# Kernel optimization log

Hardware: AMD Instinct MI355X
Metric: run time of the kernel (lower is better)

Reference implementation:

```python
import jax, jax.numpy as jnp
import numpy as np

B, T, L, M = 64, 2000, 400, 80
SIGMA_FACTOR = 0.05
SIGMA_CAP = 10.0
SIGMA_MIN = 1.5
WARMUP_STEPS = 10000
GLOBAL_STEP = 0  # fresh loss module -> progress = 0
ENTROPY_TARGET = 3.5
ATTN_W_START = 1.0
ATTN_W_MIN = 0.2
EPS = 1e-8


def setup_inputs() -> dict:
    key = jax.random.key(0)
    ks = jax.random.split(key, 8)
    mel_out_postnet = jax.random.normal(ks[0], (B, T, M), jnp.float32)
    mel_out = jax.random.normal(ks[1], (B, T, M), jnp.float32)
    gate_out = jax.random.normal(ks[2], (B, T), jnp.float32)
    # alignments: stacked per-step attention, row-normalized like real softmax outputs
    a = jax.random.uniform(ks[3], (B, T, L), jnp.float32)
    alignments = a / jnp.sum(a, axis=-1, keepdims=True)
    mel_target = jax.random.normal(ks[4], (B, T, M), jnp.float32)
    gate_target = jnp.round(jax.random.uniform(ks[5], (B, T), jnp.float32))
    mel_lengths = jax.random.randint(ks[6], (B,), T // 2, T + 1, jnp.int32).at[0].set(T)
    text_lengths = jax.random.randint(ks[7], (B,), L // 2, L + 1, jnp.int32).at[0].set(L)
    return {
        "mel_out_postnet": mel_out_postnet, "mel_out": mel_out, "gate_out": gate_out,
        "alignments": alignments, "mel_target": mel_target, "gate_target": gate_target,
        "mel_lengths": mel_lengths, "text_lengths": text_lengths,
    }


def _diagonal_target(text_lengths):
    # sigma per batch element; global_step=0 -> progress=0 -> sigma = init_sigma
    init_sigma = jnp.clip(text_lengths.astype(jnp.float32) * SIGMA_FACTOR, 3.0, SIGMA_CAP)
    progress = min(1.0, GLOBAL_STEP / float(WARMUP_STEPS))
    sigma = init_sigma - (init_sigma - SIGMA_MIN) * progress  # [B]
    t = jnp.arange(T, dtype=jnp.int32)  # decoder steps
    Lb = text_lengths[:, None]  # [B,1]
    # expected_pos = min(int(t*Lb/T), Lb-1); positive ints -> integer floor div matches trunc
    exp_pos = jnp.minimum((t[None, :] * Lb) // T, Lb - 1).astype(jnp.float32)  # [B,T]
    pos = jnp.arange(L, dtype=jnp.float32)  # [L]
    z = (pos[None, None, :] - exp_pos[:, :, None]) / sigma[:, None, None]
    g = jnp.exp(-0.5 * z * z)  # [B,T,L]
    valid = (pos[None, None, :] < text_lengths[:, None, None].astype(jnp.float32))
    g = g * valid
    return g / (jnp.sum(g, axis=-1, keepdims=True) + EPS)


def reference(mel_out_postnet, mel_out, gate_out, alignments, mel_target,
              gate_target, mel_lengths, text_lengths):
    # masked L1 on mel (mel_target already [B,T,M], matching the torch transpose)
    valid = (jnp.arange(T)[None, :] < mel_lengths[:, None])[:, :, None]  # [B,T,1]
    vf = valid.astype(jnp.float32)
    n_valid = jnp.sum(vf) * M
    mel_loss_1 = jnp.sum(jnp.abs(mel_out - mel_target) * vf) / n_valid
    mel_loss_2 = jnp.sum(jnp.abs(mel_out_postnet - mel_target) * vf) / n_valid
    loss_mel = mel_loss_1 + mel_loss_2

    # BCEWithLogits, mean reduction (stable form)
    x, z_t = gate_out, gate_target
    loss_gate = jnp.mean(jnp.maximum(x, 0.0) - x * z_t + jnp.log1p(jnp.exp(-jnp.abs(x))))

    # guided-attention KL against diagonal Gaussian target
    target = _diagonal_target(text_lengths)  # [B,T,L]
    attn_safe = jnp.maximum(alignments, EPS)
    log_pred = jnp.log(attn_safe)
    kl_pw = jnp.where(target > 0.0, target * (jnp.log(jnp.maximum(target, EPS)) - log_pred), 0.0)
    attention_kl = jnp.sum(kl_pw) / B / T  # batchmean then / T_dec
    attention_kl = jnp.minimum(attention_kl, 150.0)

    # entropy-gated attention weight (python-float in torch -> stop_gradient)
    attn_entropy = jnp.mean(-jnp.sum(attn_safe * log_pred, axis=2))
    ratio = jnp.maximum(attn_entropy / ENTROPY_TARGET, 0.0)
    weight = jnp.where(attn_entropy <= ENTROPY_TARGET,
                       jnp.maximum(ATTN_W_MIN, ATTN_W_START * ratio),
                       ATTN_W_START)
    weight = jax.lax.stop_gradient(weight)

    total_loss = loss_mel + loss_gate + weight * attention_kl
    return (total_loss, loss_mel, loss_gate, attention_kl)
```

## Files before the change

kernel.cpp:

```cpp
#include <hip/hip_runtime.h>
#include <cstddef>
#include <cstdint>

#define B_ 64
#define T_ 2000
#define L_ 400
#define M_ 80
#define EPSF 1e-8f
#define LOG2_EPSF -26.575424759098897f
#define LN2 0.6931471805599453

#define NBLK 2048
#define BT_ (B_ * T_)
#define NTHREADS (NBLK * 256)
#define NWAVES (NBLK * 4)
#define L4_ 100
#define TAIL_LANES 36
#define N4_ (B_ * T_ * (M_ / 4))
#define NCH_ (N4_ / 64)
#define MAXK 16
#define MELK 5

typedef float vf4 __attribute__((ext_vector_type(4)));

#define LOG2F(x) __builtin_amdgcn_logf(x)
#define EXP2F(x) __builtin_amdgcn_exp2f(x)

__device__ __forceinline__ float waveReduce(float v) {
#pragma unroll
  for (int m = 32; m >= 1; m >>= 1) v += __shfl_xor(v, m, 64);
  return v;
}

__global__ __launch_bounds__(256) void fused_kernel(
    const vf4* __restrict__ mo, const vf4* __restrict__ mp,
    const vf4* __restrict__ mt, const float* __restrict__ gx,
    const float* __restrict__ gz, const float* __restrict__ align,
    const int* __restrict__ mel_lengths, const int* __restrict__ text_lengths,
    double* __restrict__ ws) {
  __shared__ int sh_ml[B_];
  __shared__ int sh_tl[B_];
  if (threadIdx.x < B_) {
    sh_ml[threadIdx.x] = mel_lengths[threadIdx.x];
    sh_tl[threadIdx.x] = text_lengths[threadIdx.x];
  }
  __syncthreads();

  const int tid = blockIdx.x * 256 + threadIdx.x;
  const int lane = threadIdx.x & 63;
  const int wib = threadIdx.x >> 6;
  const int waveId = blockIdx.x * 4 + wib;

  float mel_acc = 0.f, gate_acc = 0.f, kl_acc = 0.f, ent2_acc = 0.f;

  if (tid < BT_) {
    float xv = gx[tid], z = gz[tid];
    gate_acc = fmaxf(xv, 0.f) - xv * z + log1pf(__expf(-fabsf(xv)));
  }

  const float4* a4 = reinterpret_cast<const float4*>(align);
  const float fl0 = (float)(4 * lane);

  float4 c0, c1 = make_float4(0.f, 0.f, 0.f, 0.f);
  {
    const float4* r = a4 + (size_t)waveId * L4_;
    c0 = r[lane];
    if (lane < TAIL_LANES) c1 = r[64 + lane];
  }

#pragma unroll 1
  for (int k = 0; k < MAXK; ++k) {
    const int p = waveId + k * NWAVES;
    const bool pv = (p < BT_);

    float4 n0 = make_float4(0.f, 0.f, 0.f, 0.f), n1 = n0;
    const int pn = p + NWAVES;
    if (pn < BT_) {
      const float4* r = a4 + (size_t)pn * L4_;
      n0 = r[lane];
      if (lane < TAIL_LANES) n1 = r[64 + lane];
    }

    vf4 ma, mb, md;
    int mi = 0;
    bool mv = false;
    if (k < MELK) {
      int ch = waveId + k * NWAVES;
      mv = (ch < NCH_);
      if (mv) {
        mi = ch * 64 + lane;
        ma = __builtin_nontemporal_load(&mo[mi]);
        mb = __builtin_nontemporal_load(&mp[mi]);
        md = __builtin_nontemporal_load(&mt[mi]);
      }
    }

    if (pv) {
      int b = p / T_;
      int t = p - b * T_;
      int Lb = sh_tl[b];
      float sigma = fminf(fmaxf((float)Lb * 0.05f, 3.0f), 10.0f);
      float invsig = 1.0f / sigma;
      int epi = t * Lb / T_;
      int lim = Lb - 1;
      if (epi > lim) epi = lim;
      float ep = (float)epi;
      float cg = -0.7213475204444817f * invsig * invsig;
      float d0 = fl0 - ep;
      float d1 = d0 + 256.f;

      float S = 0.f, W2 = 0.f;
      float gs[8];
#pragma unroll
      for (int j = 4; j < 8; ++j) gs[j] = 0.f;

      {
        const float av[4] = {c0.x, c0.y, c0.z, c0.w};
#pragma unroll
        for (int j = 0; j < 4; ++j) {
          float as = fmaxf(av[j], EPSF);
          float lp2 = LOG2F(as);
          ent2_acc = fmaf(-as, lp2, ent2_acc);
          float dj = d0 + (float)j;
          float e2 = dj * dj * cg;
          float gv = EXP2F(e2);
          gv = ((4 * lane + j) < Lb) ? gv : 0.f;
          gs[j] = gv;
          S += gv;
          W2 = fmaf(gv, lp2, W2);
        }
      }
      const bool c1w = (256.f - ep) < 13.6f * sigma;
      if (lane < TAIL_LANES) {
        const float av[4] = {c1.x, c1.y, c1.z, c1.w};
#pragma unroll
        for (int j = 0; j < 4; ++j) {
          float as = fmaxf(av[j], EPSF);
          float lp2 = LOG2F(as);
          ent2_acc = fmaf(-as, lp2, ent2_acc);
          if (c1w) {
            float dj = d1 + (float)j;
            float e2 = dj * dj * cg;
            float gv = EXP2F(e2);
            gv = ((256 + 4 * lane + j) < Lb) ? gv : 0.f;
            gs[4 + j] = gv;
            S += gv;
            W2 = fmaf(gv, lp2, W2);
          }
        }
      }

      float St = waveReduce(S);
      float Se = St + EPSF;
      float inv = 1.0f / Se;
      float lSe2 = LOG2F(Se);

      float K2 = 0.f;
#pragma unroll
      for (int j = 0; j < 4; ++j) {
        float dj = d0 + (float)j;
        float e2 = dj * dj * cg;
        K2 = fmaf(gs[j], fmaxf(e2 - lSe2, LOG2_EPSF), K2);
      }
      if (c1w) {
#pragma unroll
        for (int j = 0; j < 4; ++j) {
          float dj = d1 + (float)j;
          float e2 = dj * dj * cg;
          K2 = fmaf(gs[4 + j], fmaxf(e2 - lSe2, LOG2_EPSF), K2);
        }
      }
      kl_acc = fmaf(inv, K2 - W2, kl_acc);
    }

    if (mv) {
      int row = mi / 20;
      int b2 = row / T_;
      int t2 = row - b2 * T_;
      float s8 = fabsf(ma.x - md.x) + fabsf(ma.y - md.y) + fabsf(ma.z - md.z) +
                 fabsf(ma.w - md.w) + fabsf(mb.x - md.x) + fabsf(mb.y - md.y) +
                 fabsf(mb.z - md.z) + fabsf(mb.w - md.w);
      mel_acc += (t2 < sh_ml[b2]) ? s8 : 0.f;
    }

    c0 = n0;
    c1 = n1;
  }

  float w0 = waveReduce(mel_acc);
  float w1 = waveReduce(gate_acc);
  float w2 = waveReduce(kl_acc);
  float w3 = waveReduce(ent2_acc);
  __shared__ double sh[4][4];
  if (lane == 0) {
    sh[wib][0] = (double)w0; sh[wib][1] = (double)w1;
    sh[wib][2] = (double)w2; sh[wib][3] = (double)w3;
  }
  __syncthreads();
  if (threadIdx.x == 0) {
    ws[blockIdx.x]            = sh[0][0] + sh[1][0] + sh[2][0] + sh[3][0];
    ws[NBLK + blockIdx.x]     = sh[0][1] + sh[1][1] + sh[2][1] + sh[3][1];
    ws[2 * NBLK + blockIdx.x] = sh[0][2] + sh[1][2] + sh[2][2] + sh[3][2];
    ws[3 * NBLK + blockIdx.x] = sh[0][3] + sh[1][3] + sh[2][3] + sh[3][3];
  }
}

__device__ double segSum(const double* __restrict__ p, int n, double* sh) {
  double a = 0.0;
  for (int i = threadIdx.x; i < n; i += 256) a += p[i];
  sh[threadIdx.x] = a;
  __syncthreads();
  for (int s = 128; s > 0; s >>= 1) {
    if ((int)threadIdx.x < s) sh[threadIdx.x] += sh[threadIdx.x + s];
    __syncthreads();
  }
  double r = sh[0];
  __syncthreads();
  return r;
}

__global__ __launch_bounds__(256) void finalize_kernel(
    const double* __restrict__ ws, const int* __restrict__ mel_lengths,
    float* __restrict__ out) {
  __shared__ double sh[256];
  double mel_sum  = segSum(ws, NBLK, sh);
  double gate_sum = segSum(ws + NBLK, NBLK, sh);
  double kl_sum   = segSum(ws + 2 * NBLK, NBLK, sh);
  double ent_sum  = segSum(ws + 3 * NBLK, NBLK, sh);
  if (threadIdx.x == 0) {
    long nv = 0;
    for (int b = 0; b < B_; ++b) nv += mel_lengths[b];
    double n_valid = (double)nv * (double)M_;
    float loss_mel  = (float)(mel_sum / n_valid);
    float loss_gate = (float)(gate_sum / (double)(B_ * T_));
    float kl  = (float)(kl_sum * LN2 / (double)(B_ * T_));
    kl = fminf(kl, 150.0f);
    float ent = (float)(ent_sum * LN2 / (double)(B_ * T_));
    float ratio = fmaxf(ent / 3.5f, 0.0f);
    float weight = (ent <= 3.5f) ? fmaxf(0.2f, 1.0f * ratio) : 1.0f;
    out[0] = loss_mel + loss_gate + weight * kl;
    out[1] = loss_mel;
    out[2] = loss_gate;
    out[3] = kl;
  }
}

extern "C" void kernel_launch(void* const* d_in, const int* in_sizes, int n_in,
                              void* d_out, int out_size, void* d_ws, size_t ws_size,
                              hipStream_t stream) {
  const float* mel_out_postnet = (const float*)d_in[0];
  const float* mel_out         = (const float*)d_in[1];
  const float* gate_out        = (const float*)d_in[2];
  const float* alignments      = (const float*)d_in[3];
  const float* mel_target      = (const float*)d_in[4];
  const float* gate_target     = (const float*)d_in[5];
  const int*   mel_lengths     = (const int*)d_in[6];
  const int*   text_lengths    = (const int*)d_in[7];
  float* out = (float*)d_out;
  double* ws = (double*)d_ws;

  fused_kernel<<<dim3(NBLK), dim3(256), 0, stream>>>(
      (const vf4*)mel_out, (const vf4*)mel_out_postnet,
      (const vf4*)mel_target, gate_out, gate_target,
      alignments, mel_lengths, text_lengths, ws);
  finalize_kernel<<<dim3(1), dim3(256), 0, stream>>>(ws, mel_lengths, out);
}
```

Measured before the change: 386.1 us.

## Process attention rows in pairs and skip masked mel rows per batch

The attention loop now handles two rows per iteration, with two independent compute streams, a combined wave reduction and prefetch of both next rows, to give more instruction-level parallelism and hide shuffle latency. Mel loss work is remapped so each group of 128 waves covers one batch element and only loads rows within mel_length, so the memory traffic for masked frames is skipped. Per-batch sigma constants and the window threshold are precomputed in shared memory, and nontemporal loads are dropped. Processing two rows at once raises register pressure, and the mel coverage relies on 5 iterations of 128 waves reaching every valid row.

```diff
diff --git a/kernel.cpp b/kernel.cpp
--- a/kernel.cpp
+++ b/kernel.cpp
@@ -12,16 +12,13 @@
 
 #define NBLK 2048
 #define BT_ (B_ * T_)
-#define NTHREADS (NBLK * 256)
-#define NWAVES (NBLK * 4)
+#define NW_ (NBLK * 4)
+#define PAIRS 8
+#define PSTRIDE (2 * NW_)
 #define L4_ 100
 #define TAIL_LANES 36
-#define N4_ (B_ * T_ * (M_ / 4))
-#define NCH_ (N4_ / 64)
-#define MAXK 16
-#define MELK 5
-
-typedef float vf4 __attribute__((ext_vector_type(4)));
+#define MELW 128
+#define MELB4 (T_ * (M_ / 4))
 
 #define LOG2F(x) __builtin_amdgcn_logf(x)
 #define EXP2F(x) __builtin_amdgcn_exp2f(x)
@@ -32,17 +29,34 @@
   return v;
 }
 
+__device__ __forceinline__ void waveReduce2(float& a, float& b) {
+#pragma unroll
+  for (int m = 32; m >= 1; m >>= 1) {
+    float ta = __shfl_xor(a, m, 64);
+    float tb = __shfl_xor(b, m, 64);
+    a += ta;
+    b += tb;
+  }
+}
+
 __global__ __launch_bounds__(256) void fused_kernel(
-    const vf4* __restrict__ mo, const vf4* __restrict__ mp,
-    const vf4* __restrict__ mt, const float* __restrict__ gx,
+    const float4* __restrict__ mo, const float4* __restrict__ mp,
+    const float4* __restrict__ mt, const float* __restrict__ gx,
     const float* __restrict__ gz, const float* __restrict__ align,
     const int* __restrict__ mel_lengths, const int* __restrict__ text_lengths,
     double* __restrict__ ws) {
-  __shared__ int sh_ml[B_];
   __shared__ int sh_tl[B_];
+  __shared__ int sh_bound[B_];
+  __shared__ float sh_cg[B_];
+  __shared__ float sh_thr[B_];
   if (threadIdx.x < B_) {
-    sh_ml[threadIdx.x] = mel_lengths[threadIdx.x];
-    sh_tl[threadIdx.x] = text_lengths[threadIdx.x];
+    int tl = text_lengths[threadIdx.x];
+    sh_tl[threadIdx.x] = tl;
+    sh_bound[threadIdx.x] = mel_lengths[threadIdx.x] * (M_ / 4);
+    float sigma = fminf(fmaxf((float)tl * 0.05f, 3.0f), 10.0f);
+    float invsig = 1.0f / sigma;
+    sh_cg[threadIdx.x] = -0.7213475204444817f * invsig * invsig;
+    sh_thr[threadIdx.x] = 256.0f - 13.6f * sigma;
   }
   __syncthreads();
 
@@ -58,133 +72,159 @@
     gate_acc = fmaxf(xv, 0.f) - xv * z + log1pf(__expf(-fabsf(xv)));
   }
 
+  const int b_mel = waveId >> 7;
+  const int melq = waveId & (MELW - 1);
+  const int melBound = sh_bound[b_mel];
+  const float4* melBaseO = mo + (size_t)b_mel * MELB4;
+  const float4* melBaseP = mp + (size_t)b_mel * MELB4;
+  const float4* melBaseT = mt + (size_t)b_mel * MELB4;
+
   const float4* a4 = reinterpret_cast<const float4*>(align);
   const float fl0 = (float)(4 * lane);
-
-  float4 c0, c1 = make_float4(0.f, 0.f, 0.f, 0.f);
-  {
-    const float4* r = a4 + (size_t)waveId * L4_;
-    c0 = r[lane];
-    if (lane < TAIL_LANES) c1 = r[64 + lane];
-  }
-
-#pragma unroll 1
-  for (int k = 0; k < MAXK; ++k) {
-    const int p = waveId + k * NWAVES;
-    const bool pv = (p < BT_);
-
-    float4 n0 = make_float4(0.f, 0.f, 0.f, 0.f), n1 = n0;
-    const int pn = p + NWAVES;
-    if (pn < BT_) {
-      const float4* r = a4 + (size_t)pn * L4_;
-      n0 = r[lane];
-      if (lane < TAIL_LANES) n1 = r[64 + lane];
-    }
-
-    vf4 ma, mb, md;
-    int mi = 0;
-    bool mv = false;
-    if (k < MELK) {
-      int ch = waveId + k * NWAVES;
-      mv = (ch < NCH_);
-      if (mv) {
-        mi = ch * 64 + lane;
-        ma = __builtin_nontemporal_load(&mo[mi]);
-        mb = __builtin_nontemporal_load(&mp[mi]);
-        md = __builtin_nontemporal_load(&mt[mi]);
-      }
-    }
-
-    if (pv) {
-      int b = p / T_;
-      int t = p - b * T_;
-      int Lb = sh_tl[b];
-      float sigma = fminf(fmaxf((float)Lb * 0.05f, 3.0f), 10.0f);
-      float invsig = 1.0f / sigma;
-      int epi = t * Lb / T_;
-      int lim = Lb - 1;
-      if (epi > lim) epi = lim;
-      float ep = (float)epi;
-      float cg = -0.7213475204444817f * invsig * invsig;
-      float d0 = fl0 - ep;
-      float d1 = d0 + 256.f;
-
-      float S = 0.f, W2 = 0.f;
-      float gs[8];
-#pragma unroll
-      for (int j = 4; j < 8; ++j) gs[j] = 0.f;
-
-      {
-        const float av[4] = {c0.x, c0.y, c0.z, c0.w};
-#pragma unroll
-        for (int j = 0; j < 4; ++j) {
-          float as = fmaxf(av[j], EPSF);
-          float lp2 = LOG2F(as);
-          ent2_acc = fmaf(-as, lp2, ent2_acc);
-          float dj = d0 + (float)j;
+  const float4 f4z = make_float4(0.f, 0.f, 0.f, 0.f);
+
+  float gsA[8], gsB[8];
+
+  auto pass1 = [&](int p, const float4& r0, const float4& r1, float* gs,
+                   float& S, float& W2, float& d0, float& cg, int& Lb,
+                   bool& c1w) {
+    int b = p / T_;
+    int t = p - b * T_;
+    Lb = sh_tl[b];
+    cg = sh_cg[b];
+    int epi = t * Lb / T_;
+    int lim = Lb - 1;
+    if (epi > lim) epi = lim;
+    float ep = (float)epi;
+    c1w = ep > sh_thr[b];
+    d0 = fl0 - ep;
+    S = 0.f;
+    W2 = 0.f;
+    const float a0[4] = {r0.x, r0.y, r0.z, r0.w};
+#pragma unroll
+    for (int j = 0; j < 4; ++j) {
+      float as = fmaxf(a0[j], EPSF);
+      float lp2 = LOG2F(as);
+      ent2_acc = fmaf(-as, lp2, ent2_acc);
+      float dj = d0 + (float)j;
+      float e2 = dj * dj * cg;
+      float gv = EXP2F(e2);
+      gv = ((4 * lane + j) < Lb) ? gv : 0.f;
+      gs[j] = gv;
+      S += gv;
+      W2 = fmaf(gv, lp2, W2);
+    }
+    if (lane < TAIL_LANES) {
+      const float a1[4] = {r1.x, r1.y, r1.z, r1.w};
+#pragma unroll
+      for (int j = 0; j < 4; ++j) {
+        float as = fmaxf(a1[j], EPSF);
+        float lp2 = LOG2F(as);
+        ent2_acc = fmaf(-as, lp2, ent2_acc);
+        float gv = 0.f;
+        if (c1w) {
+          float dj = d0 + 256.f + (float)j;
           float e2 = dj * dj * cg;
-          float gv = EXP2F(e2);
-          gv = ((4 * lane + j) < Lb) ? gv : 0.f;
-          gs[j] = gv;
+          gv = EXP2F(e2);
+          gv = ((256 + 4 * lane + j) < Lb) ? gv : 0.f;
           S += gv;
           W2 = fmaf(gv, lp2, W2);
         }
+        gs[4 + j] = gv;
       }
-      const bool c1w = (256.f - ep) < 13.6f * sigma;
-      if (lane < TAIL_LANES) {
-        const float av[4] = {c1.x, c1.y, c1.z, c1.w};
-#pragma unroll
-        for (int j = 0; j < 4; ++j) {
-          float as = fmaxf(av[j], EPSF);
-          float lp2 = LOG2F(as);
-          ent2_acc = fmaf(-as, lp2, ent2_acc);
-          if (c1w) {
-            float dj = d1 + (float)j;
-            float e2 = dj * dj * cg;
-            float gv = EXP2F(e2);
-            gv = ((256 + 4 * lane + j) < Lb) ? gv : 0.f;
-            gs[4 + j] = gv;
-            S += gv;
-            W2 = fmaf(gv, lp2, W2);
-          }
-        }
+    } else {
+#pragma unroll
+      for (int j = 0; j < 4; ++j) gs[4 + j] = 0.f;
+    }
+  };
+
+  auto pass2 = [&](const float* gs, float d0, float cg, float S, float W2,
+                   bool c1w) {
+    float Se = S + EPSF;
+    float inv = 1.0f / Se;
+    float lSe2 = LOG2F(Se);
+    float K2 = 0.f;
+#pragma unroll
+    for (int j = 0; j < 4; ++j) {
+      float dj = d0 + (float)j;
+      float e2 = dj * dj * cg;
+      K2 = fmaf(gs[j], fmaxf(e2 - lSe2, LOG2_EPSF), K2);
+    }
+    if (c1w) {
+#pragma unroll
+      for (int j = 0; j < 4; ++j) {
+        float dj = d0 + 256.f + (float)j;
+        float e2 = dj * dj * cg;
+        K2 = fmaf(gs[4 + j], fmaxf(e2 - lSe2, LOG2_EPSF), K2);
       }
-
-      float St = waveReduce(S);
-      float Se = St + EPSF;
-      float inv = 1.0f / Se;
-      float lSe2 = LOG2F(Se);
-
-      float K2 = 0.f;
-#pragma unroll
-      for (int j = 0; j < 4; ++j) {
-        float dj = d0 + (float)j;
-        float e2 = dj * dj * cg;
-        K2 = fmaf(gs[j], fmaxf(e2 - lSe2, LOG2_EPSF), K2);
+    }
+    kl_acc = fmaf(inv, K2 - W2, kl_acc);
+  };
+
+  float4 a0, a1 = f4z, b0, b1 = f4z;
+  {
+    const float4* r = a4 + (size_t)waveId * L4_;
+    a0 = r[lane];
+    if (lane < TAIL_LANES) a1 = r[64 + lane];
+    const float4* r2 = a4 + (size_t)(waveId + NW_) * L4_;
+    b0 = r2[lane];
+    if (lane < TAIL_LANES) b1 = r2[64 + lane];
+  }
+
+#pragma unroll 1
+  for (int kp = 0; kp < PAIRS; ++kp) {
+    const int pA = waveId + kp * PSTRIDE;
+    const int pB = pA + NW_;
+    const bool bv = (pB < BT_);
+
+    float SA, W2A, d0A, cgA;
+    int LbA;
+    bool cwA;
+    pass1(pA, a0, a1, gsA, SA, W2A, d0A, cgA, LbA, cwA);
+
+    float4 na0 = f4z, na1 = f4z, nb0 = f4z, nb1 = f4z;
+    const int qA = pA + PSTRIDE;
+    if (kp + 1 < PAIRS) {
+      const float4* r = a4 + (size_t)qA * L4_;
+      na0 = r[lane];
+      if (lane < TAIL_LANES) na1 = r[64 + lane];
+    }
+
+    float SB = 0.f, W2B = 0.f, d0B = 0.f, cgB = 0.f;
+    int LbB = 0;
+    bool cwB = false;
+    if (bv) pass1(pB, b0, b1, gsB, SB, W2B, d0B, cgB, LbB, cwB);
+
+    const int qB = qA + NW_;
+    if (kp + 1 < PAIRS && qB < BT_) {
+      const float4* r = a4 + (size_t)qB * L4_;
+      nb0 = r[lane];
+      if (lane < TAIL_LANES) nb1 = r[64 + lane];
+    }
+
+    float4 ma, mb, md;
+    bool mv = false;
+    if (kp < 5) {
+      int i = melq * 64 + lane + kp * (MELW * 64);
+      mv = (i < melBound);
+      if (mv) {
+        ma = melBaseO[i];
+        mb = melBaseP[i];
+        md = melBaseT[i];
       }
-      if (c1w) {
-#pragma unroll
-        for (int j = 0; j < 4; ++j) {
-          float dj = d1 + (float)j;
-          float e2 = dj * dj * cg;
-          K2 = fmaf(gs[4 + j], fmaxf(e2 - lSe2, LOG2_EPSF), K2);
-        }
-      }
-      kl_acc = fmaf(inv, K2 - W2, kl_acc);
-    }
+    }
+
+    waveReduce2(SA, SB);
+    pass2(gsA, d0A, cgA, SA, W2A, cwA);
+    if (bv) pass2(gsB, d0B, cgB, SB, W2B, cwB);
 
     if (mv) {
-      int row = mi / 20;
-      int b2 = row / T_;
-      int t2 = row - b2 * T_;
-      float s8 = fabsf(ma.x - md.x) + fabsf(ma.y - md.y) + fabsf(ma.z - md.z) +
+      mel_acc += fabsf(ma.x - md.x) + fabsf(ma.y - md.y) + fabsf(ma.z - md.z) +
                  fabsf(ma.w - md.w) + fabsf(mb.x - md.x) + fabsf(mb.y - md.y) +
                  fabsf(mb.z - md.z) + fabsf(mb.w - md.w);
-      mel_acc += (t2 < sh_ml[b2]) ? s8 : 0.f;
-    }
-
-    c0 = n0;
-    c1 = n1;
+    }
+
+    a0 = na0; a1 = na1; b0 = nb0; b1 = nb1;
   }
 
   float w0 = waveReduce(mel_acc);
@@ -223,13 +263,15 @@
     const double* __restrict__ ws, const int* __restrict__ mel_lengths,
     float* __restrict__ out) {
   __shared__ double sh[256];
+  __shared__ int sh_nv[64];
+  if (threadIdx.x < B_) sh_nv[threadIdx.x] = mel_lengths[threadIdx.x];
   double mel_sum  = segSum(ws, NBLK, sh);
   double gate_sum = segSum(ws + NBLK, NBLK, sh);
   double kl_sum   = segSum(ws + 2 * NBLK, NBLK, sh);
   double ent_sum  = segSum(ws + 3 * NBLK, NBLK, sh);
   if (threadIdx.x == 0) {
     long nv = 0;
-    for (int b = 0; b < B_; ++b) nv += mel_lengths[b];
+    for (int b = 0; b < B_; ++b) nv += sh_nv[b];
     double n_valid = (double)nv * (double)M_;
     float loss_mel  = (float)(mel_sum / n_valid);
     float loss_gate = (float)(gate_sum / (double)(B_ * T_));
@@ -260,8 +302,8 @@
   double* ws = (double*)d_ws;
 
   fused_kernel<<<dim3(NBLK), dim3(256), 0, stream>>>(
-      (const vf4*)mel_out, (const vf4*)mel_out_postnet,
-      (const vf4*)mel_target, gate_out, gate_target,
+      (const float4*)mel_out, (const float4*)mel_out_postnet,
+      (const float4*)mel_target, gate_out, gate_target,
       alignments, mel_lengths, text_lengths, ws);
   finalize_kernel<<<dim3(1), dim3(256), 0, stream>>>(ws, mel_lengths, out);
 }
```

New measurement: 378.0 us. 2.1% less time.
